# Kernel optimization log

Hardware: AMD Instinct MI355X
Metric: run time of the kernel (lower is better)

Reference implementation:

```python
import jax, jax.numpy as jnp
import numpy as np

NUM_HEADS = 12


def _rel_indices(H, W):
    # [N, N, 3] with channels (dx, dy, dx^2+dy^2), N = H*W
    indx = jnp.arange(W)[None, :] - jnp.arange(W)[:, None]          # [W, W]
    indx = jnp.tile(indx, (H, H))                                    # [N, N]
    indy = jnp.arange(H)[None, :] - jnp.arange(H)[:, None]          # [H, H]
    indy = jnp.repeat(jnp.repeat(indy, W, axis=0), W, axis=1)        # [N, N]
    indd = indx ** 2 + indy ** 2
    return jnp.stack([indx, indy, indd], axis=-1).astype(jnp.float32)


def setup_inputs() -> dict:
    key = jax.random.key(0)
    ks = jax.random.split(key, 8)
    B, N, C = 16, 576, 768
    std = 0.02
    return {
        "x": jax.random.normal(ks[0], (B, N, C), dtype=jnp.float32),
        "Wq": jax.random.normal(ks[1], (C, C), dtype=jnp.float32) * std,
        "Wk": jax.random.normal(ks[2], (C, C), dtype=jnp.float32) * std,
        "Wv": jax.random.normal(ks[3], (C, C), dtype=jnp.float32) * std,
        "Wproj": jax.random.normal(ks[4], (C, C), dtype=jnp.float32) * std,
        "bproj": jnp.zeros((C,), dtype=jnp.float32),
        "pos_w": jax.random.normal(ks[5], (3, NUM_HEADS), dtype=jnp.float32) * std,
        "pos_b": jnp.zeros((NUM_HEADS,), dtype=jnp.float32),
        "gating": jnp.ones((NUM_HEADS,), dtype=jnp.float32),
        "H": 24,
        "W": 24,
    }


def reference(x, Wq, Wk, Wv, Wproj, bproj, pos_w, pos_b, gating, H, W):
    B, N, C = x.shape
    h = gating.shape[0]
    d = C // h
    scale = d ** (-0.5)

    def heads(t):  # [B,N,C] -> [B,h,N,d]
        return t.reshape(B, N, h, d).transpose(0, 2, 1, 3)

    q = heads(x @ Wq)
    k = heads(x @ Wk)
    v = heads(x @ Wv)

    # content scores: [B,h,N,N]
    patch_score = jax.nn.softmax(jnp.einsum('bhnd,bhmd->bhnm', q, k) * scale, axis=-1)

    # positional scores: shared across batch, [h,N,N]
    rel = _rel_indices(H, W)                      # [N,N,3]
    pos_score = jnp.einsum('nmc,ch->hnm', rel, pos_w) + pos_b[:, None, None]
    pos_score = jax.nn.softmax(pos_score, axis=-1)

    gate = jax.nn.sigmoid(gating)[None, :, None, None]  # [1,h,1,1]
    attn = (1.0 - gate) * patch_score + gate * pos_score[None]
    attn = attn / jnp.sum(attn, axis=-1, keepdims=True)

    out = jnp.einsum('bhnm,bhmd->bhnd', attn, v)         # [B,h,N,d]
    out = out.transpose(0, 2, 1, 3).reshape(B, N, C)
    return out @ Wproj + bproj
```

## Files before the change

kernel.cpp:

```cpp
#include <hip/hip_runtime.h>
#include <math.h>

#define B_ 16
#define N_ 576
#define C_ 768
#define NH 12
#define D_ 64
#define STR 68
#define QKV 2304

typedef unsigned short u16;
typedef __bf16 bf16x8 __attribute__((ext_vector_type(8)));
typedef float f32x4 __attribute__((ext_vector_type(4)));

__device__ __forceinline__ u16 f2bf(float f) {
    unsigned u = __builtin_bit_cast(unsigned, f);
    unsigned r = (u + 0x7FFFu + ((u >> 16) & 1u)) >> 16;
    return (u16)r;
}

__device__ __forceinline__ bf16x8 ldsF8u(const u16* p) {
    union { uint2 u[2]; bf16x8 v; } t;
    t.u[0] = *(const uint2*)p;
    t.u[1] = *(const uint2*)(p + 4);
    return t.v;
}
__device__ __forceinline__ bf16x8 ldsF8a(const u16* p) {
    union { uint4 u; bf16x8 v; } t;
    t.u = *(const uint4*)p;
    return t.v;
}

__device__ __forceinline__ void gload16(const u16* g, u16* l) {
    __builtin_amdgcn_global_load_lds(
        (const __attribute__((address_space(1))) void*)g,
        (__attribute__((address_space(3))) void*)l,
        16, 0, 0);
}

__global__ __launch_bounds__(256)
void conv_x_kernel(const float* __restrict__ x, u16* __restrict__ xb)
{
    int i = blockIdx.x * 256 + threadIdx.x;
    float4 v = ((const float4*)x)[i];
    u16 o[4] = {f2bf(v.x), f2bf(v.y), f2bf(v.z), f2bf(v.w)};
    *(uint2*)&xb[(size_t)i * 4] = *(const uint2*)o;
}

__global__ __launch_bounds__(256)
void transpose_w_kernel(const float* __restrict__ src, u16* __restrict__ dst)
{
    __shared__ float t[32][33];
    const int bx = blockIdx.x * 32, by = blockIdx.y * 32;
    const int tx = threadIdx.x & 31, ty = threadIdx.x >> 5;
#pragma unroll
    for (int i = 0; i < 32; i += 8)
        t[ty + i][tx] = src[(size_t)(by + ty + i) * C_ + bx + tx];
    __syncthreads();
#pragma unroll
    for (int i = 0; i < 32; i += 8)
        dst[(size_t)(bx + ty + i) * C_ + by + tx] = f2bf(t[tx][ty + i]);
}

__global__ __launch_bounds__(256)
void transpose_v_kernel(const u16* __restrict__ qkvb, u16* __restrict__ vtb)
{
    __shared__ u16 t[64 * 72];
    const int n0 = blockIdx.x * 64;
    const int bh = blockIdx.y;
    const int b = bh / NH, h = bh % NH;
    const int tid = threadIdx.x;
    const u16* src = qkvb + ((size_t)b * N_ + n0) * QKV + 2 * C_ + h * D_;
#pragma unroll
    for (int p = 0; p < 2; ++p) {
        int idx = p * 256 + tid;
        int r = idx >> 3, c = (idx & 7) << 3;
        *(uint4*)&t[r * 72 + c] = *(const uint4*)(src + (size_t)r * QKV + c);
    }
    __syncthreads();
    u16* dst = vtb + (size_t)bh * D_ * N_ + n0;
#pragma unroll
    for (int p = 0; p < 2; ++p) {
        int idx = p * 256 + tid;
        int dd = idx >> 3, n8 = (idx & 7) << 3;
        u16 o[8];
#pragma unroll
        for (int j = 0; j < 8; ++j) o[j] = t[(n8 + j) * 72 + dd];
        *(uint4*)(dst + (size_t)dd * N_ + n8) = *(const uint4*)o;
    }
}

__global__ __launch_bounds__(256)
void mfma_gemm(const u16* __restrict__ A,
               const u16* __restrict__ BT,
               const float* __restrict__ bias,
               float* __restrict__ out,
               u16* __restrict__ outb,
               int ldo, int mode)
{
    const int K = C_;
    __shared__ __align__(16) u16 As[128 * 64];
    __shared__ __align__(16) u16 Bs[128 * 64];
    const int tid = threadIdx.x;
    const int wave = tid >> 6, lane = tid & 63;
    const int quad = lane >> 4, l16 = lane & 15;
    const int wy = wave >> 1, wx = wave & 1;
    const int tm = blockIdx.y * 128, tn = blockIdx.x * 128;

    const int lr = lane >> 3;
    const int sc = ((lane & 7) ^ lr) * 8;

    f32x4 acc[4][4];
#pragma unroll
    for (int i = 0; i < 4; ++i)
#pragma unroll
        for (int j = 0; j < 4; ++j)
            acc[i][j] = (f32x4){0.f, 0.f, 0.f, 0.f};

    for (int k0 = 0; k0 < K; k0 += 64) {
        __syncthreads();
#pragma unroll
        for (int t = 0; t < 4; ++t) {
            const int rg = wave * 32 + t * 8;
            gload16(A  + (size_t)(tm + rg + lr) * K + k0 + sc, &As[rg * 64]);
            gload16(BT + (size_t)(tn + rg + lr) * K + k0 + sc, &Bs[rg * 64]);
        }
        __syncthreads();

#pragma unroll
        for (int kh = 0; kh < 2; ++kh) {
            bf16x8 aA[4], bB[4];
#pragma unroll
            for (int i = 0; i < 4; ++i) {
                const int s = (kh * 4 + quad) ^ (l16 & 7);
                aA[i] = ldsF8a(&As[(wy * 64 + i * 16 + l16) * 64 + s * 8]);
            }
#pragma unroll
            for (int j = 0; j < 4; ++j) {
                const int s = (kh * 4 + quad) ^ (l16 & 7);
                bB[j] = ldsF8a(&Bs[(wx * 64 + j * 16 + l16) * 64 + s * 8]);
            }
#pragma unroll
            for (int i = 0; i < 4; ++i)
#pragma unroll
                for (int j = 0; j < 4; ++j)
                    acc[i][j] = __builtin_amdgcn_mfma_f32_16x16x32_bf16(aA[i], bB[j], acc[i][j], 0, 0, 0);
        }
    }

    if (mode == 0) {
#pragma unroll
        for (int i = 0; i < 4; ++i) {
#pragma unroll
            for (int r = 0; r < 4; ++r) {
                const int m = tm + wy * 64 + i * 16 + quad * 4 + r;
#pragma unroll
                for (int j = 0; j < 4; ++j) {
                    const int c = tn + wx * 64 + j * 16 + l16;
                    out[(size_t)m * ldo + c] = acc[i][j][r] + bias[c];
                }
            }
        }
    } else {
        const float scale = (tn < C_) ? 0.125f : 1.0f;
#pragma unroll
        for (int i = 0; i < 4; ++i) {
#pragma unroll
            for (int r = 0; r < 4; ++r) {
                const int m = tm + wy * 64 + i * 16 + quad * 4 + r;
#pragma unroll
                for (int j = 0; j < 4; ++j) {
                    const int c = tn + wx * 64 + j * 16 + l16;
                    outb[(size_t)m * ldo + c] = f2bf(acc[i][j][r] * scale);
                }
            }
        }
    }
}

__global__ __launch_bounds__(256)
void pos_softmax_kernel(const float* __restrict__ pos_w,
                        const float* __restrict__ pos_b,
                        const int* __restrict__ Hp,
                        const int* __restrict__ Wp,
                        u16* __restrict__ pos_out)
{
    const int n = blockIdx.x;
    const int hh = blockIdx.y;
    const int tid = threadIdx.x;
    __shared__ float srow[N_];
    __shared__ float wred[4];
    const int Ww = Wp[0];
    (void)Hp;
    const float w0 = pos_w[0 * NH + hh];
    const float w1 = pos_w[1 * NH + hh];
    const float w2 = pos_w[2 * NH + hh];
    const float bb = pos_b[hh];
    const int nx = n % Ww, ny = n / Ww;

    float lmax = -1e30f;
    for (int m = tid; m < N_; m += 256) {
        float dx = (float)((m % Ww) - nx);
        float dy = (float)((m / Ww) - ny);
        float sc = dx * w0 + dy * w1 + (dx * dx + dy * dy) * w2 + bb;
        srow[m] = sc;
        lmax = fmaxf(lmax, sc);
    }
#pragma unroll
    for (int off = 32; off; off >>= 1) lmax = fmaxf(lmax, __shfl_down(lmax, off, 64));
    if ((tid & 63) == 0) wred[tid >> 6] = lmax;
    __syncthreads();
    float M = fmaxf(fmaxf(wred[0], wred[1]), fmaxf(wred[2], wred[3]));
    __syncthreads();

    float lsum = 0.f;
    for (int m = tid; m < N_; m += 256) {
        float e = __expf(srow[m] - M);
        srow[m] = e;
        lsum += e;
    }
#pragma unroll
    for (int off = 32; off; off >>= 1) lsum += __shfl_down(lsum, off, 64);
    if ((tid & 63) == 0) wred[tid >> 6] = lsum;
    __syncthreads();
    float inv = 1.0f / (wred[0] + wred[1] + wred[2] + wred[3]);

    u16* op = pos_out + ((size_t)hh * N_ + n) * N_;
    for (int m = tid; m < N_; m += 256) op[m] = f2bf(srow[m] * inv);
}

__global__ __launch_bounds__(256)
void attn_kernel(const u16* __restrict__ qkvb,
                 const u16* __restrict__ vt,
                 const u16* __restrict__ pos,
                 const float* __restrict__ gating,
                 u16* __restrict__ ao)
{
    const int qt = blockIdx.x;
    const int bh = blockIdx.y;
    const int b = bh / NH, h = bh % NH;
    const int tid = threadIdx.x;
    const int wave = tid >> 6, lane = tid & 63;
    const int quad = lane >> 4, l16 = lane & 15;

    __shared__ u16 smem[4 * 64 * STR];
    u16* Kt = smem;
    u16* Vs = smem + 64 * STR;
    u16* Pp = smem + 2 * 64 * STR;
    u16* Pb = smem + 3 * 64 * STR;

    const u16* qptr  = qkvb + ((size_t)b * N_ + qt * 64) * QKV + h * D_;
    const u16* kbase = qkvb + (size_t)b * N_ * QKV + C_ + h * D_;
    const u16* vbase = vt + (size_t)bh * D_ * N_;
    const u16* pbase = pos + ((size_t)h * N_ + qt * 64) * N_;

    const int sr = tid >> 3;
    const int scol = (tid & 7) << 3;

#pragma unroll
    for (int p = 0; p < 2; ++p) {
        int r = p * 32 + sr;
        uint4 d = *(const uint4*)(qptr + (size_t)r * QKV + scol);
        *(uint2*)&Pb[r * STR + scol]     = make_uint2(d.x, d.y);
        *(uint2*)&Pb[r * STR + scol + 4] = make_uint2(d.z, d.w);
    }
    __syncthreads();

    const int arow = wave * 16 + l16;
    bf16x8 aq0 = ldsF8u(&Pb[arow * STR + quad * 8]);
    bf16x8 aq1 = ldsF8u(&Pb[arow * STR + 32 + quad * 8]);

    uint4 rk[2], rv[2], rp[2];
    auto loadT = [&](int m0) {
#pragma unroll
        for (int p = 0; p < 2; ++p) {
            int r = p * 32 + sr;
            rk[p] = *(const uint4*)(kbase + (size_t)(m0 + r) * QKV + scol);
            rv[p] = *(const uint4*)(vbase + (size_t)r * N_ + m0 + scol);
            rp[p] = *(const uint4*)(pbase + (size_t)r * N_ + m0 + scol);
        }
    };
    auto writeT = [&]() {
#pragma unroll
        for (int p = 0; p < 2; ++p) {
            int r = p * 32 + sr;
            *(uint2*)&Kt[r * STR + scol]     = make_uint2(rk[p].x, rk[p].y);
            *(uint2*)&Kt[r * STR + scol + 4] = make_uint2(rk[p].z, rk[p].w);
            *(uint2*)&Vs[r * STR + scol]     = make_uint2(rv[p].x, rv[p].y);
            *(uint2*)&Vs[r * STR + scol + 4] = make_uint2(rv[p].z, rv[p].w);
            *(uint2*)&Pp[r * STR + scol]     = make_uint2(rp[p].x, rp[p].y);
            *(uint2*)&Pp[r * STR + scol + 4] = make_uint2(rp[p].z, rp[p].w);
        }
    };

    loadT(0);

    f32x4 oc[4], op[4];
#pragma unroll
    for (int nt = 0; nt < 4; ++nt) {
        oc[nt] = (f32x4){0.f, 0.f, 0.f, 0.f};
        op[nt] = (f32x4){0.f, 0.f, 0.f, 0.f};
    }
    float lrun[4] = {0.f, 0.f, 0.f, 0.f};

    for (int mt = 0; mt < 9; ++mt) {
        __syncthreads();
        writeT();
        __syncthreads();
        if (mt < 8) loadT((mt + 1) * 64);

        f32x4 s[4];
#pragma unroll
        for (int nt = 0; nt < 4; ++nt) {
            bf16x8 b0 = ldsF8u(&Kt[(nt * 16 + l16) * STR + quad * 8]);
            bf16x8 b1 = ldsF8u(&Kt[(nt * 16 + l16) * STR + 32 + quad * 8]);
            f32x4 z = (f32x4){0.f, 0.f, 0.f, 0.f};
            z = __builtin_amdgcn_mfma_f32_16x16x32_bf16(aq0, b0, z, 0, 0, 0);
            z = __builtin_amdgcn_mfma_f32_16x16x32_bf16(aq1, b1, z, 0, 0, 0);
            s[nt] = z;
        }

#pragma unroll
        for (int r = 0; r < 4; ++r) {
            const int prow = (wave * 16 + quad * 4 + r) * STR;
            float e0 = __expf(s[0][r]);
            float e1 = __expf(s[1][r]);
            float e2 = __expf(s[2][r]);
            float e3 = __expf(s[3][r]);
            Pb[prow +  0 + l16] = f2bf(e0);
            Pb[prow + 16 + l16] = f2bf(e1);
            Pb[prow + 32 + l16] = f2bf(e2);
            Pb[prow + 48 + l16] = f2bf(e3);
            lrun[r] += (e0 + e1) + (e2 + e3);
        }
        asm volatile("s_waitcnt lgkmcnt(0)" ::: "memory");

#pragma unroll
        for (int ks = 0; ks < 2; ++ks) {
            bf16x8 ap   = ldsF8u(&Pb[arow * STR + ks * 32 + quad * 8]);
            bf16x8 apos = ldsF8u(&Pp[arow * STR + ks * 32 + quad * 8]);
#pragma unroll
            for (int nt = 0; nt < 4; ++nt) {
                bf16x8 bv = ldsF8u(&Vs[(nt * 16 + l16) * STR + ks * 32 + quad * 8]);
                oc[nt] = __builtin_amdgcn_mfma_f32_16x16x32_bf16(ap,   bv, oc[nt], 0, 0, 0);
                op[nt] = __builtin_amdgcn_mfma_f32_16x16x32_bf16(apos, bv, op[nt], 0, 0, 0);
            }
        }
    }

#pragma unroll
    for (int r = 0; r < 4; ++r) {
        lrun[r] += __shfl_xor(lrun[r], 1, 64);
        lrun[r] += __shfl_xor(lrun[r], 2, 64);
        lrun[r] += __shfl_xor(lrun[r], 4, 64);
        lrun[r] += __shfl_xor(lrun[r], 8, 64);
    }

    const float g = 1.f / (1.f + __expf(-gating[h]));
#pragma unroll
    for (int r = 0; r < 4; ++r) {
        const float sc = (1.f - g) / lrun[r];
        const int row = qt * 64 + wave * 16 + quad * 4 + r;
#pragma unroll
        for (int nt = 0; nt < 4; ++nt) {
            ao[((size_t)b * N_ + row) * C_ + h * D_ + nt * 16 + l16] =
                f2bf(oc[nt][r] * sc + g * op[nt][r]);
        }
    }
}

extern "C" void kernel_launch(void* const* d_in, const int* in_sizes, int n_in,
                              void* d_out, int out_size, void* d_ws, size_t ws_size,
                              hipStream_t stream)
{
    const float* x      = (const float*)d_in[0];
    const float* Wq     = (const float*)d_in[1];
    const float* Wk     = (const float*)d_in[2];
    const float* Wv     = (const float*)d_in[3];
    const float* Wproj  = (const float*)d_in[4];
    const float* bproj  = (const float*)d_in[5];
    const float* pos_w  = (const float*)d_in[6];
    const float* pos_b  = (const float*)d_in[7];
    const float* gating = (const float*)d_in[8];
    const int*   Hp     = (const int*)d_in[9];
    const int*   Wp     = (const int*)d_in[10];
    float* out = (float*)d_out;

    const size_t xe = (size_t)B_ * N_ * C_;
    const size_t we = (size_t)C_ * C_;
    const size_t qe = (size_t)B_ * N_ * QKV;
    const size_t pe = (size_t)NH * N_ * N_;
    u16* xb   = (u16*)d_ws;
    u16* wt   = xb + xe;
    u16* wtp  = wt + 3 * we;
    u16* qkvb = wtp + we;
    u16* vtb  = qkvb + qe;
    u16* posb = vtb + xe;
    u16* aob  = posb + pe;
    size_t need = (size_t)(3 * xe + 4 * we + qe + pe) * sizeof(u16);
    if (ws_size < need) return;

    conv_x_kernel<<<dim3((unsigned)(xe / 1024)), 256, 0, stream>>>(x, xb);
    dim3 tgrid(24, 24);
    transpose_w_kernel<<<tgrid, 256, 0, stream>>>(Wq, wt);
    transpose_w_kernel<<<tgrid, 256, 0, stream>>>(Wk, wt + we);
    transpose_w_kernel<<<tgrid, 256, 0, stream>>>(Wv, wt + 2 * we);
    transpose_w_kernel<<<tgrid, 256, 0, stream>>>(Wproj, wtp);

    mfma_gemm<<<dim3(18, 72), 256, 0, stream>>>(xb, wt, nullptr, nullptr,
                                                qkvb, QKV, 1);
    transpose_v_kernel<<<dim3(9, B_ * NH), 256, 0, stream>>>(qkvb, vtb);
    pos_softmax_kernel<<<dim3(N_, NH), 256, 0, stream>>>(pos_w, pos_b, Hp, Wp, posb);
    attn_kernel<<<dim3(9, B_ * NH), 256, 0, stream>>>(qkvb, vtb, posb, gating, aob);
    mfma_gemm<<<dim3(6, 72), 256, 0, stream>>>(aob, wtp, bproj, out,
                                               nullptr, C_, 0);
}
```

Before: 248.0 us.

## Replace QKV GEMM with 256x256-tile, 8-wave, double-buffered pipelined MFMA kernel

The QKV projection moves to a new GEMM using 256x256 output tiles with 512 threads. It double-buffers A and B tiles in 128 KB of LDS, interleaving the global-to-LDS staging of the next k-tile with MFMA phases under barriers and s_setprio. It also remaps workgroups across XCDs for locality and uses an XOR-swizzled LDS layout. The aim is more operand reuse and better overlap of memory with compute, at the cost of heavy register and LDS use, which lowers occupancy, and only 324 workgroups for the grid.

Result: faster. 242.8 us (-2.1%).

```diff
diff --git a/kernel.cpp b/kernel.cpp
--- a/kernel.cpp
+++ b/kernel.cpp
@@ -173,6 +173,138 @@
                     const int c = tn + wx * 64 + j * 16 + l16;
                     outb[(size_t)m * ldo + c] = f2bf(acc[i][j][r] * scale);
                 }
+            }
+        }
+    }
+}
+
+__device__ __forceinline__ void stage_half256(const u16* __restrict__ g,
+                                              int grow0, int k0,
+                                              u16* lds, int wave, int lane)
+{
+    const int lr = lane >> 3;
+    const int sc = ((lane & 7) ^ lr) * 8;
+#pragma unroll
+    for (int l = 0; l < 2; ++l) {
+        const int r = l * 64 + wave * 8;
+        gload16(g + (size_t)(grow0 + r + lr) * C_ + k0 + sc, lds + r * 64);
+    }
+}
+
+__global__ __launch_bounds__(512, 2)
+void mfma_gemm256(const u16* __restrict__ A,
+                  const u16* __restrict__ BT,
+                  u16* __restrict__ outb)
+{
+    __shared__ __align__(16) u16 sm[2][2][256 * 64];
+    const int tid = threadIdx.x;
+    const int wave = tid >> 6, lane = tid & 63;
+    const int quad = lane >> 4, l16 = lane & 15;
+    const int wr = wave >> 2, wc = wave & 3;
+
+    const int gx = gridDim.x;
+    const int nwg = gx * gridDim.y;
+    const int o = blockIdx.y * gx + blockIdx.x;
+    const int q8 = nwg >> 3, r8 = nwg & 7;
+    const int xcd = o & 7, idx = o >> 3;
+    const int wg = (xcd < r8 ? xcd * (q8 + 1) : r8 * (q8 + 1) + (xcd - r8) * q8) + idx;
+    const int tm = (wg / gx) * 256;
+    const int tn = (wg % gx) * 256;
+
+    f32x4 acc[8][4];
+#pragma unroll
+    for (int i = 0; i < 8; ++i)
+#pragma unroll
+        for (int j = 0; j < 4; ++j)
+            acc[i][j] = (f32x4){0.f, 0.f, 0.f, 0.f};
+
+    stage_half256(A,  tm,       0,  sm[0][0],            wave, lane);
+    stage_half256(A,  tm + 128, 0,  sm[0][0] + 128 * 64, wave, lane);
+    stage_half256(BT, tn,       0,  sm[0][1],            wave, lane);
+    stage_half256(BT, tn + 128, 0,  sm[0][1] + 128 * 64, wave, lane);
+    stage_half256(BT, tn,       64, sm[1][1],            wave, lane);
+    stage_half256(BT, tn + 128, 64, sm[1][1] + 128 * 64, wave, lane);
+    asm volatile("s_waitcnt vmcnt(4)" ::: "memory");
+    __builtin_amdgcn_s_barrier();
+
+    auto ktile = [&](int u, u16* Acur, u16* Bcur, u16* Anxt, u16* Bnxt) {
+        const int k1 = (u + 1) * 64, k2 = (u + 2) * 64;
+        bf16x8 bb[4][2];
+        bf16x8 af[2][2];
+
+#pragma unroll
+        for (int j = 0; j < 4; ++j)
+#pragma unroll
+            for (int kh = 0; kh < 2; ++kh)
+                bb[j][kh] = ldsF8a(&Bcur[(wc * 64 + j * 16 + l16) * 64 +
+                                         (((kh * 4 + quad) ^ (l16 & 7)) * 8)]);
+#pragma unroll
+        for (int t = 0; t < 2; ++t)
+#pragma unroll
+            for (int kh = 0; kh < 2; ++kh)
+                af[t][kh] = ldsF8a(&Acur[(wr * 128 + t * 16 + l16) * 64 +
+                                         (((kh * 4 + quad) ^ (l16 & 7)) * 8)]);
+        asm volatile("" ::: "memory");
+        if (u < 11) stage_half256(A, tm, k1, Anxt, wave, lane);
+        __builtin_amdgcn_s_barrier();
+        __builtin_amdgcn_s_setprio(1);
+#pragma unroll
+        for (int t = 0; t < 2; ++t)
+#pragma unroll
+            for (int j = 0; j < 4; ++j)
+#pragma unroll
+                for (int kh = 0; kh < 2; ++kh)
+                    acc[t][j] = __builtin_amdgcn_mfma_f32_16x16x32_bf16(
+                        af[t][kh], bb[j][kh], acc[t][j], 0, 0, 0);
+        __builtin_amdgcn_s_setprio(0);
+        __builtin_amdgcn_s_barrier();
+
+#pragma unroll
+        for (int ph = 1; ph < 4; ++ph) {
+#pragma unroll
+            for (int t = 0; t < 2; ++t)
+#pragma unroll
+                for (int kh = 0; kh < 2; ++kh)
+                    af[t][kh] = ldsF8a(&Acur[(wr * 128 + (ph * 2 + t) * 16 + l16) * 64 +
+                                             (((kh * 4 + quad) ^ (l16 & 7)) * 8)]);
+            asm volatile("" ::: "memory");
+            if (ph == 1)      { if (u < 11) stage_half256(A,  tm + 128, k1, Anxt + 128 * 64, wave, lane); }
+            else if (ph == 2) { if (u < 10) stage_half256(BT, tn,       k2, Bcur,            wave, lane); }
+            else              { if (u < 10) stage_half256(BT, tn + 128, k2, Bcur + 128 * 64, wave, lane); }
+            __builtin_amdgcn_s_barrier();
+            __builtin_amdgcn_s_setprio(1);
+#pragma unroll
+            for (int t = 0; t < 2; ++t)
+#pragma unroll
+                for (int j = 0; j < 4; ++j)
+#pragma unroll
+                    for (int kh = 0; kh < 2; ++kh)
+                        acc[ph * 2 + t][j] = __builtin_amdgcn_mfma_f32_16x16x32_bf16(
+                            af[t][kh], bb[j][kh], acc[ph * 2 + t][j], 0, 0, 0);
+            __builtin_amdgcn_s_setprio(0);
+            if (ph == 3) {
+                if (u < 10)       asm volatile("s_waitcnt vmcnt(4)" ::: "memory");
+                else if (u == 10) asm volatile("s_waitcnt vmcnt(0)" ::: "memory");
+            }
+            __builtin_amdgcn_s_barrier();
+        }
+    };
+
+    for (int uu = 0; uu < 12; uu += 2) {
+        ktile(uu,     sm[0][0], sm[0][1], sm[1][0], sm[1][1]);
+        ktile(uu + 1, sm[1][0], sm[1][1], sm[0][0], sm[0][1]);
+    }
+
+    const float scale = (tn < C_) ? 0.125f : 1.0f;
+#pragma unroll
+    for (int i = 0; i < 8; ++i) {
+#pragma unroll
+        for (int r = 0; r < 4; ++r) {
+            const int m = tm + wr * 128 + i * 16 + quad * 4 + r;
+#pragma unroll
+            for (int j = 0; j < 4; ++j) {
+                const int c = tn + wc * 64 + j * 16 + l16;
+                outb[(size_t)m * QKV + c] = f2bf(acc[i][j][r] * scale);
             }
         }
     }
@@ -407,8 +539,7 @@
     transpose_w_kernel<<<tgrid, 256, 0, stream>>>(Wv, wt + 2 * we);
     transpose_w_kernel<<<tgrid, 256, 0, stream>>>(Wproj, wtp);
 
-    mfma_gemm<<<dim3(18, 72), 256, 0, stream>>>(xb, wt, nullptr, nullptr,
-                                                qkvb, QKV, 1);
+    mfma_gemm256<<<dim3(9, 36), 512, 0, stream>>>(xb, wt, qkvb);
     transpose_v_kernel<<<dim3(9, B_ * NH), 256, 0, stream>>>(qkvb, vtb);
     pos_softmax_kernel<<<dim3(N_, NH), 256, 0, stream>>>(pos_w, pos_b, Hp, Wp, posb);
     attn_kernel<<<dim3(9, B_ * NH), 256, 0, stream>>>(qkvb, vtb, posb, gating, aob);
```

## Swizzle attention LDS tiles for 128-bit loads and remap GEMM block order

Applied to the files above, without the earlier changes.

Replaces the padded stride-68 LDS layout in the attention kernel with an XOR-swizzled 64-wide layout. This lets K, V, Q and positional tiles be written and read with single 16-byte LDS operations instead of pairs of 8-byte ones while avoiding bank conflicts. The GEMM kernel also remaps workgroup IDs so consecutive blocks are spread across eight groups, likely to improve cache locality across XCDs. The V transpose kernel moves to stride-68 padding with split 8-byte stores. The remap assumes the workgroup count is divisible by eight, and the swizzle costs some extra index arithmetic.

New measurement: 344.6 us. +38.9%, slower.

```diff
diff --git a/kernel.cpp b/kernel.cpp
--- a/kernel.cpp
+++ b/kernel.cpp
@@ -6,7 +6,6 @@
 #define C_ 768
 #define NH 12
 #define D_ 64
-#define STR 68
 #define QKV 2304
 
 typedef unsigned short u16;
@@ -19,16 +18,14 @@
     return (u16)r;
 }
 
-__device__ __forceinline__ bf16x8 ldsF8u(const u16* p) {
-    union { uint2 u[2]; bf16x8 v; } t;
-    t.u[0] = *(const uint2*)p;
-    t.u[1] = *(const uint2*)(p + 4);
-    return t.v;
-}
 __device__ __forceinline__ bf16x8 ldsF8a(const u16* p) {
     union { uint4 u; bf16x8 v; } t;
     t.u = *(const uint4*)p;
     return t.v;
+}
+
+__device__ __forceinline__ int asw(int r, int c) {
+    return r * 64 + ((((c >> 3) ^ r) & 7) << 3) + (c & 7);
 }
 
 __device__ __forceinline__ void gload16(const u16* g, u16* l) {
@@ -65,7 +62,7 @@
 __global__ __launch_bounds__(256)
 void transpose_v_kernel(const u16* __restrict__ qkvb, u16* __restrict__ vtb)
 {
-    __shared__ u16 t[64 * 72];
+    __shared__ u16 t[64 * 68];
     const int n0 = blockIdx.x * 64;
     const int bh = blockIdx.y;
     const int b = bh / NH, h = bh % NH;
@@ -75,7 +72,9 @@
     for (int p = 0; p < 2; ++p) {
         int idx = p * 256 + tid;
         int r = idx >> 3, c = (idx & 7) << 3;
-        *(uint4*)&t[r * 72 + c] = *(const uint4*)(src + (size_t)r * QKV + c);
+        uint4 d = *(const uint4*)(src + (size_t)r * QKV + c);
+        *(uint2*)&t[r * 68 + c]     = make_uint2(d.x, d.y);
+        *(uint2*)&t[r * 68 + c + 4] = make_uint2(d.z, d.w);
     }
     __syncthreads();
     u16* dst = vtb + (size_t)bh * D_ * N_ + n0;
@@ -85,7 +84,7 @@
         int dd = idx >> 3, n8 = (idx & 7) << 3;
         u16 o[8];
 #pragma unroll
-        for (int j = 0; j < 8; ++j) o[j] = t[(n8 + j) * 72 + dd];
+        for (int j = 0; j < 8; ++j) o[j] = t[(n8 + j) * 68 + dd];
         *(uint4*)(dst + (size_t)dd * N_ + n8) = *(const uint4*)o;
     }
 }
@@ -105,7 +104,12 @@
     const int wave = tid >> 6, lane = tid & 63;
     const int quad = lane >> 4, l16 = lane & 15;
     const int wy = wave >> 1, wx = wave & 1;
-    const int tm = blockIdx.y * 128, tn = blockIdx.x * 128;
+
+    const int gx = gridDim.x;
+    const int nwg = gx * gridDim.y;
+    int o = blockIdx.y * gx + blockIdx.x;
+    o = (o & 7) * (nwg >> 3) + (o >> 3);
+    const int tm = (o / gx) * 128, tn = (o % gx) * 128;
 
     const int lr = lane >> 3;
     const int sc = ((lane & 7) ^ lr) * 8;
@@ -243,11 +247,11 @@
     const int wave = tid >> 6, lane = tid & 63;
     const int quad = lane >> 4, l16 = lane & 15;
 
-    __shared__ u16 smem[4 * 64 * STR];
+    __shared__ __align__(16) u16 smem[4 * 64 * 64];
     u16* Kt = smem;
-    u16* Vs = smem + 64 * STR;
-    u16* Pp = smem + 2 * 64 * STR;
-    u16* Pb = smem + 3 * 64 * STR;
+    u16* Vs = smem + 64 * 64;
+    u16* Pp = smem + 2 * 64 * 64;
+    u16* Pb = smem + 3 * 64 * 64;
 
     const u16* qptr  = qkvb + ((size_t)b * N_ + qt * 64) * QKV + h * D_;
     const u16* kbase = qkvb + (size_t)b * N_ * QKV + C_ + h * D_;
@@ -261,14 +265,13 @@
     for (int p = 0; p < 2; ++p) {
         int r = p * 32 + sr;
         uint4 d = *(const uint4*)(qptr + (size_t)r * QKV + scol);
-        *(uint2*)&Pb[r * STR + scol]     = make_uint2(d.x, d.y);
-        *(uint2*)&Pb[r * STR + scol + 4] = make_uint2(d.z, d.w);
+        *(uint4*)&Pb[asw(r, scol)] = d;
     }
     __syncthreads();
 
     const int arow = wave * 16 + l16;
-    bf16x8 aq0 = ldsF8u(&Pb[arow * STR + quad * 8]);
-    bf16x8 aq1 = ldsF8u(&Pb[arow * STR + 32 + quad * 8]);
+    bf16x8 aq0 = ldsF8a(&Pb[asw(arow, quad * 8)]);
+    bf16x8 aq1 = ldsF8a(&Pb[asw(arow, 32 + quad * 8)]);
 
     uint4 rk[2], rv[2], rp[2];
     auto loadT = [&](int m0) {
@@ -284,12 +287,9 @@
 #pragma unroll
         for (int p = 0; p < 2; ++p) {
             int r = p * 32 + sr;
-            *(uint2*)&Kt[r * STR + scol]     = make_uint2(rk[p].x, rk[p].y);
-            *(uint2*)&Kt[r * STR + scol + 4] = make_uint2(rk[p].z, rk[p].w);
-            *(uint2*)&Vs[r * STR + scol]     = make_uint2(rv[p].x, rv[p].y);
-            *(uint2*)&Vs[r * STR + scol + 4] = make_uint2(rv[p].z, rv[p].w);
-            *(uint2*)&Pp[r * STR + scol]     = make_uint2(rp[p].x, rp[p].y);
-            *(uint2*)&Pp[r * STR + scol + 4] = make_uint2(rp[p].z, rp[p].w);
+            *(uint4*)&Kt[asw(r, scol)] = rk[p];
+            *(uint4*)&Vs[asw(r, scol)] = rv[p];
+            *(uint4*)&Pp[asw(r, scol)] = rp[p];
         }
     };
 
@@ -312,8 +312,8 @@
         f32x4 s[4];
 #pragma unroll
         for (int nt = 0; nt < 4; ++nt) {
-            bf16x8 b0 = ldsF8u(&Kt[(nt * 16 + l16) * STR + quad * 8]);
-            bf16x8 b1 = ldsF8u(&Kt[(nt * 16 + l16) * STR + 32 + quad * 8]);
+            bf16x8 b0 = ldsF8a(&Kt[asw(nt * 16 + l16, quad * 8)]);
+            bf16x8 b1 = ldsF8a(&Kt[asw(nt * 16 + l16, 32 + quad * 8)]);
             f32x4 z = (f32x4){0.f, 0.f, 0.f, 0.f};
             z = __builtin_amdgcn_mfma_f32_16x16x32_bf16(aq0, b0, z, 0, 0, 0);
             z = __builtin_amdgcn_mfma_f32_16x16x32_bf16(aq1, b1, z, 0, 0, 0);
@@ -322,26 +322,26 @@
 
 #pragma unroll
         for (int r = 0; r < 4; ++r) {
-            const int prow = (wave * 16 + quad * 4 + r) * STR;
+            const int prow = wave * 16 + quad * 4 + r;
             float e0 = __expf(s[0][r]);
             float e1 = __expf(s[1][r]);
             float e2 = __expf(s[2][r]);
             float e3 = __expf(s[3][r]);
-            Pb[prow +  0 + l16] = f2bf(e0);
-            Pb[prow + 16 + l16] = f2bf(e1);
-            Pb[prow + 32 + l16] = f2bf(e2);
-            Pb[prow + 48 + l16] = f2bf(e3);
+            Pb[asw(prow, l16)]      = f2bf(e0);
+            Pb[asw(prow, 16 + l16)] = f2bf(e1);
+            Pb[asw(prow, 32 + l16)] = f2bf(e2);
+            Pb[asw(prow, 48 + l16)] = f2bf(e3);
             lrun[r] += (e0 + e1) + (e2 + e3);
         }
         asm volatile("s_waitcnt lgkmcnt(0)" ::: "memory");
 
 #pragma unroll
         for (int ks = 0; ks < 2; ++ks) {
-            bf16x8 ap   = ldsF8u(&Pb[arow * STR + ks * 32 + quad * 8]);
-            bf16x8 apos = ldsF8u(&Pp[arow * STR + ks * 32 + quad * 8]);
+            bf16x8 ap   = ldsF8a(&Pb[asw(arow, ks * 32 + quad * 8)]);
+            bf16x8 apos = ldsF8a(&Pp[asw(arow, ks * 32 + quad * 8)]);
 #pragma unroll
             for (int nt = 0; nt < 4; ++nt) {
-                bf16x8 bv = ldsF8u(&Vs[(nt * 16 + l16) * STR + ks * 32 + quad * 8]);
+                bf16x8 bv = ldsF8a(&Vs[asw(nt * 16 + l16, ks * 32 + quad * 8)]);
                 oc[nt] = __builtin_amdgcn_mfma_f32_16x16x32_bf16(ap,   bv, oc[nt], 0, 0, 0);
                 op[nt] = __builtin_amdgcn_mfma_f32_16x16x32_bf16(apos, bv, op[nt], 0, 0, 0);
             }
```
